# Optimization experiments

Measured on AMD Instinct MI355X. Metric: run time of the kernel, lower is better.

The kernel has to match this reference:

```python
import jax, jax.numpy as jnp
import numpy as np

N_SITES = 1024
CHI = 128


def _cayley_isometry(X):
    # X: (m, n) with m >= n. Pad to square, skew-symmetrize, Cayley transform
    # Q = (I + A)^{-1}(I - A) (orthogonal for skew A), keep first n columns
    # -> isometry with orthonormal columns (quimb isometrize(method='cayley')).
    m, n = X.shape
    S = jnp.zeros((m, m), X.dtype).at[:, :n].set(X)
    A = 0.5 * (S - S.T)
    I = jnp.eye(m, dtype=X.dtype)
    Q = jnp.linalg.solve(I + A, I - A)
    return Q[:, :n]


def setup_inputs() -> dict:
    key = jax.random.key(0)
    k1, k2 = jax.random.split(key)
    params = jax.random.normal(k1, (N_SITES, 2 * CHI, CHI), jnp.float32) * 0.1
    rand_uniform = jax.random.uniform(k2, (N_SITES,), dtype=jnp.float32)
    return {"params": params, "rand_uniform": rand_uniform}


def reference(params, rand_uniform):
    n, two_chi, chi = params.shape
    # norm_fn: isometrize every TN tensor via Cayley, reshape to (left,2,right)
    W = jax.vmap(_cayley_isometry)(params)          # (N, 2*chi, chi)
    T = W.reshape(n, chi, 2, chi)
    l = jnp.zeros((chi,), W.dtype).at[0].set(1.0)   # left boundary vector
    r = jnp.zeros((chi,), W.dtype).at[0].set(1.0)   # right boundary vector

    # right environments of <psi|psi>: Rs[i] contracts sites i..N-1
    def right_step(R, Ti):
        Rn = jnp.einsum('asb,csd,bd->ac', Ti, Ti, R)
        return Rn, Rn

    R_last = jnp.outer(r, r)
    _, Rs = jax.lax.scan(right_step, R_last, T, reverse=True)
    # env strictly to the right of site i
    R_right = jnp.concatenate([Rs[1:], R_last[None]], axis=0)  # (N, chi, chi)

    # global normalization so conditional probs satisfy ps0+ps1 = 1
    L0 = jnp.outer(l, l)
    Z = jnp.einsum('ab,ab->', L0, Rs[0])
    T = T.at[0].multiply(jax.lax.rsqrt(Z))

    def sample_step(L, inp):
        Ti, Ri, u = inp
        # reduced density matrix on this site's physical index k_i
        rho = jnp.einsum('ab,asc,btd,cd->st', L, Ti, Ti, Ri)
        ps0 = rho[1, 1]   # <v0|rho|v0>, v0 = [0, 1]
        ps1 = rho[0, 0]   # <v1|rho|v1>, v1 = [1, 0]
        take0 = u < ps0
        vec = jnp.where(take0,
                        jnp.array([0.0, 1.0], rho.dtype),
                        jnp.array([1.0, 0.0], rho.dtype))
        p = jnp.where(take0, ps0, ps1)
        # project site on sampled vector, renormalize by its probability
        M = jnp.einsum('asb,s->ab', Ti, vec)
        Ln = jnp.einsum('ab,ac,bd->cd', L, M, M) / p
        return N_ if False else (Ln, vec)

    _, s_hat = jax.lax.scan(sample_step, L0, (T, R_right, rand_uniform))
    return s_hat  # (N, 2) float32, rows are v0=[0,1] or v1=[1,0]
```

## Files before the change

kernel.cpp:

```cpp
#include <hip/hip_runtime.h>
#include <math.h>

#define NS 1024
#define SENT (-1.0e300)

template <typename T> struct V2;
template <> struct V2<double> { using t = double2; };
template <> struct V2<float>  { using t = float2; };

template <typename T> __device__ __forceinline__ T sentv();
template <> __device__ __forceinline__ double sentv<double>() { return -1.0e300; }
template <> __device__ __forceinline__ float  sentv<float>()  { return -3.0e38f; }

template <typename T>
__device__ __forceinline__ T aldT(const T* p) {
  return __hip_atomic_load(p, __ATOMIC_RELAXED, __HIP_MEMORY_SCOPE_AGENT);
}
__device__ __forceinline__ double ald(const double* p) {
  return __hip_atomic_load(p, __ATOMIC_RELAXED, __HIP_MEMORY_SCOPE_AGENT);
}
template <typename T>
__device__ __forceinline__ void ast(T* p, T v) {
  __hip_atomic_store(p, v, __ATOMIC_RELAXED, __HIP_MEMORY_SCOPE_AGENT);
}

template <typename TR>
__global__ void k_init(double* __restrict__ wbuf, TR* __restrict__ Rbuf) {
  size_t stride = (size_t)gridDim.x * blockDim.x;
  size_t t = (size_t)blockIdx.x * blockDim.x + threadIdx.x;
  for (size_t idx = t; idx < (size_t)(NS + 1) * 128; idx += stride)
    wbuf[idx] = (idx < 128) ? ((idx == 0) ? 1.0 : 0.0) : SENT;
  const size_t lastoff = (size_t)(NS - 1) * 16384;
  for (size_t idx = t; idx < (size_t)NS * 16384; idx += stride)
    Rbuf[idx] = (idx < lastoff) ? sentv<TR>()
                                : (TR)((idx == lastoff) ? 1.0f : 0.0f);
}

template <typename TT, typename TR>
__global__ __launch_bounds__(256) void k_cayley(const float* __restrict__ params,
                                                TT* __restrict__ Tk,
                                                TR* __restrict__ Yscr) {
  __shared__ float XB[64 * 132];
  __shared__ double prow[128], fcol[128];
  const int site = blockIdx.x, tid = threadIdx.x;
  const float* X = params + (size_t)site * 256 * 128;
  const int ti = tid >> 4, tj = tid & 15;
  const int R0 = ti * 8, C0 = tj * 8;
  double g[8][8];
  #pragma unroll
  for (int i = 0; i < 8; ++i)
    #pragma unroll
    for (int j = 0; j < 8; ++j) g[i][j] = ((R0 + i) == (C0 + j)) ? 1.0 : 0.0;
  for (int h = 0; h < 2; ++h) {
    for (int idx = tid; idx < 64 * 128; idx += 256) {
      int rr = idx >> 7, c = idx & 127;
      XB[rr * 132 + c] = X[(size_t)(h * 64 + rr) * 128 + c];
    }
    __syncthreads();
    int lo = h * 64;
    if ((R0 >> 6) == h) {
      #pragma unroll
      for (int i = 0; i < 8; ++i)
        #pragma unroll
        for (int j = 0; j < 8; ++j)
          g[i][j] += 0.5 * (double)XB[(R0 + i - lo) * 132 + (C0 + j)];
    }
    if ((C0 >> 6) == h) {
      #pragma unroll
      for (int i = 0; i < 8; ++i)
        #pragma unroll
        for (int j = 0; j < 8; ++j)
          g[i][j] -= 0.5 * (double)XB[(C0 + j - lo) * 132 + (R0 + i)];
    }
    __syncthreads();
  }
  for (int h = 0; h < 2; ++h) {
    for (int idx = tid; idx < 64 * 128; idx += 256) {
      int rr = idx >> 7, c = idx & 127;
      XB[rr * 132 + c] = X[(size_t)(128 + h * 64 + rr) * 128 + c];
    }
    __syncthreads();
    for (int a = 0; a < 64; ++a) {
      double fa[8], fb[8];
      #pragma unroll
      for (int i = 0; i < 8; ++i) fa[i] = 0.5 * (double)XB[a * 132 + R0 + i];
      #pragma unroll
      for (int j = 0; j < 8; ++j) fb[j] = 0.5 * (double)XB[a * 132 + C0 + j];
      #pragma unroll
      for (int i = 0; i < 8; ++i)
        #pragma unroll
        for (int j = 0; j < 8; ++j) g[i][j] += fa[i] * fb[j];
    }
    __syncthreads();
  }
  for (int p = 0; p < 128; ++p) {
    int pb = p >> 3, pl = p & 7;
    if (ti == pb) {
      #pragma unroll
      for (int j = 0; j < 8; ++j) prow[C0 + j] = g[pl][j];
    }
    if (tj == pb) {
      #pragma unroll
      for (int i = 0; i < 8; ++i) fcol[R0 + i] = g[i][pl];
    }
    __syncthreads();
    double d = 1.0 / prow[p];
    double pd[8];
    #pragma unroll
    for (int j = 0; j < 8; ++j) pd[j] = prow[C0 + j] * d;
    #pragma unroll
    for (int i = 0; i < 8; ++i) {
      int r = R0 + i;
      if (r == p) {
        #pragma unroll
        for (int j = 0; j < 8; ++j) g[i][j] = ((C0 + j) == p) ? d : pd[j];
      } else {
        double f = fcol[r];
        #pragma unroll
        for (int j = 0; j < 8; ++j)
          g[i][j] = ((C0 + j) == p) ? (-f * d) : (g[i][j] - f * pd[j]);
      }
    }
    __syncthreads();
  }
  TR* Ys = Yscr + (size_t)site * 16384;
  TT* Ts = Tk + (size_t)site * 32768;
  #pragma unroll
  for (int i = 0; i < 8; ++i) {
    int r = R0 + i, s = r & 1, a = r >> 1;
    #pragma unroll
    for (int j = 0; j < 8; ++j) {
      int c = C0 + j;
      Ys[(size_t)r * 128 + c] = (TR)g[i][j];
      Ts[((size_t)s * 128 + a) * 128 + c] =
          (TT)(2.0 * g[i][j] - ((r == c) ? 1.0 : 0.0));
    }
  }
}

template <typename TT, typename TR>
__global__ __launch_bounds__(256) void k_w2(const float* __restrict__ params,
                                            const TR* __restrict__ Yscr,
                                            TT* __restrict__ Tk) {
  __shared__ float X2c[16 * 132];
  __shared__ double Yt[16 * 130];
  const int site = blockIdx.x, tid = threadIdx.x;
  const float* X2g = params + (size_t)site * 256 * 128 + 128 * 128;
  const TR* Ys = Yscr + (size_t)site * 16384;
  TT* Ts = Tk + (size_t)site * 32768;
  const int ti = tid >> 4, tj = tid & 15;
  const int R0 = ti * 8, C0 = tj * 8;
  double acc[8][8];
  #pragma unroll
  for (int i = 0; i < 8; ++i)
    #pragma unroll
    for (int j = 0; j < 8; ++j) acc[i][j] = 0.0;
  for (int b0 = 0; b0 < 128; b0 += 16) {
    __syncthreads();
    for (int idx = tid; idx < 2048; idx += 256) {
      int r = idx >> 4, bb = idx & 15;
      X2c[bb * 132 + r] = X2g[(size_t)r * 128 + b0 + bb];
    }
    for (int idx = tid; idx < 2048; idx += 256) {
      int bb = idx >> 7, c = idx & 127;
      Yt[bb * 130 + c] = (double)Ys[(size_t)(b0 + bb) * 128 + c];
    }
    __syncthreads();
    for (int bb = 0; bb < 16; ++bb) {
      double xf[8], yf[8];
      #pragma unroll
      for (int i = 0; i < 8; ++i) xf[i] = (double)X2c[bb * 132 + R0 + i];
      #pragma unroll
      for (int j = 0; j < 8; ++j) yf[j] = Yt[bb * 130 + C0 + j];
      #pragma unroll
      for (int i = 0; i < 8; ++i)
        #pragma unroll
        for (int j = 0; j < 8; ++j) acc[i][j] += xf[i] * yf[j];
    }
  }
  #pragma unroll
  for (int i = 0; i < 8; ++i) {
    int r = 128 + R0 + i, s = r & 1, a = r >> 1;
    #pragma unroll
    for (int j = 0; j < 8; ++j)
      Ts[((size_t)s * 128 + a) * 128 + C0 + j] = (TT)(-acc[i][j]);
  }
}

template <typename TT, typename TR>
__global__ __launch_bounds__(512) void k_scan(const TT* __restrict__ Tk,
                                              TR* __restrict__ Rbuf,
                                              TR* __restrict__ Rs0,
                                              double* __restrict__ Zp) {
  __shared__ double KA[8 * 128];
  __shared__ double KC[16 * 129];
  __shared__ double Rt[16 * 128];
  __shared__ double Pb[8 * 129];
  __shared__ double red[256];
  const int w = blockIdx.x, tid = threadIdx.x;
  const int a0 = (w >> 3) * 4, c0 = (w & 7) * 16;
  const int r2 = tid >> 7, bh = tid & 127;
  const TR SV = sentv<TR>();
  for (int i = NS - 1; i >= 0; --i) {
    const TT* K = Tk + (size_t)i * 32768;
    const TR* Rin = Rbuf + (size_t)i * 16384;
    double v[4];
    #pragma unroll
    for (int u = 0; u < 4; ++u) {
      TR t = aldT(Rin + tid * 4 + u);
      v[u] = (t == SV) ? SENT : (double)t;
    }
    for (int idx = tid; idx < 1024; idx += 512) {
      int row = idx >> 7, col = idx & 127;
      KA[idx] = (double)K[(size_t)((row >> 2) * 128 + a0 + (row & 3)) * 128 + col];
    }
    double kc[8];
    #pragma unroll
    for (int u = 0; u < 8; ++u) {
      int row = r2 + 4 * u;
      kc[u] = (double)K[(size_t)((row >> 4) * 128 + c0 + (row & 15)) * 128 + bh];
    }
    double acc0 = 0.0, acc1 = 0.0;
    for (int c = 0; c < 8; ++c) {
      while (v[0] == SENT || v[1] == SENT || v[2] == SENT || v[3] == SENT) {
        __builtin_amdgcn_s_sleep(1);
        #pragma unroll
        for (int u = 0; u < 4; ++u)
          if (v[u] == SENT) {
            TR t = aldT(Rin + c * 2048 + tid * 4 + u);
            v[u] = (t == SV) ? SENT : (double)t;
          }
      }
      {
        int base = tid * 4, dl = base >> 7, bb = base & 127;
        Rt[dl * 128 + bb] = v[0];
        Rt[dl * 128 + bb + 1] = v[1];
        Rt[dl * 128 + bb + 2] = v[2];
        Rt[dl * 128 + bb + 3] = v[3];
      }
      __syncthreads();
      if (c < 7) {
        #pragma unroll
        for (int u = 0; u < 4; ++u) {
          TR t = aldT(Rin + (c + 1) * 2048 + tid * 4 + u);
          v[u] = (t == SV) ? SENT : (double)t;
        }
      }
      #pragma unroll
      for (int dl = 0; dl < 16; ++dl) {
        int d = c * 16 + dl;
        double rr = Rt[dl * 128 + bh];
        acc0 += KA[r2 * 128 + d] * rr;
        acc1 += KA[(r2 + 4) * 128 + d] * rr;
      }
      __syncthreads();
    }
    Pb[r2 * 129 + bh] = acc0;
    Pb[(r2 + 4) * 129 + bh] = acc1;
    __syncthreads();
    double s = 0.0;
    const int oi = tid & 63, seg = (tid >> 6) & 3;
    #pragma unroll
    for (int j = 0; j < 2; ++j) {
      #pragma unroll
      for (int t = 0; t < 4; ++t)
        KC[(r2 + 4 * t) * 129 + bh] = kc[j * 4 + t];
      __syncthreads();
      if (tid < 256) {
        int aa = oi >> 4, cc = oi & 15;
        double acc = 0.0;
        #pragma unroll
        for (int m = 0; m < 32; ++m) {
          int b = seg * 32 + m;
          acc += Pb[(j * 4 + aa) * 129 + b] * KC[cc * 129 + b];
        }
        s += acc;
      }
      __syncthreads();
    }
    if (tid < 256) red[tid] = s;
    __syncthreads();
    if (tid < 64) {
      int aa = tid >> 4, cc = tid & 15;
      double o = red[tid] + red[tid + 64] + red[tid + 128] + red[tid + 192];
      TR* outp = (i > 0) ? (Rbuf + (size_t)(i - 1) * 16384) : Rs0;
      ast(&outp[(size_t)(a0 + aa) * 128 + c0 + cc], (TR)o);
      if (i == 0 && w == 0 && tid == 0) ast(Zp, o);
    }
    __syncthreads();
  }
}

template <typename TT, typename TR>
__global__ __launch_bounds__(1024) void k_sample(const TT* __restrict__ Tk,
                                                 const TR* __restrict__ Rbuf,
                                                 double* __restrict__ wbuf,
                                                 const double* __restrict__ Zp,
                                                 const float* __restrict__ randu,
                                                 float* __restrict__ out) {
  __shared__ double wl[128], yl[256], part[1024], ctrl[2];
  const int g = blockIdx.x, tid = threadIdx.x;
  const int s = tid >> 9, q = (tid >> 7) & 3, b = tid & 127;
  const int lane = tid & 63, wv = tid >> 6;
  using TR2 = typename V2<TR>::t;
  for (int site = g; site < NS; site += 16) {
    const TT* T = Tk + (size_t)site * 32768;
    double tf[32];
    {
      const TT* tp = T + ((size_t)s * 128 + q * 32) * 128 + b;
      #pragma unroll
      for (int t = 0; t < 32; ++t) tf[t] = (double)tp[(size_t)t * 128];
    }
    double rv[16];
    {
      const TR2* R2 = (const TR2*)(Rbuf + (size_t)site * 16384);
      #pragma unroll
      for (int t = 0; t < 8; ++t) {
        TR2 v = R2[t * 1024 + tid];
        rv[2 * t] = (double)v.x; rv[2 * t + 1] = (double)v.y;
      }
    }
    if (tid < 128) {
      double* wp = wbuf + (size_t)site * 128 + tid;
      double v;
      while ((v = ald(wp)) == SENT) __builtin_amdgcn_s_sleep(1);
      wl[tid] = v;
    }
    __syncthreads();
    {
      double p0 = 0.0;
      #pragma unroll
      for (int t = 0; t < 32; ++t) p0 += tf[t] * wl[q * 32 + t];
      part[(s * 4 + q) * 128 + b] = p0;
    }
    __syncthreads();
    if (tid < 256) {
      int ss = tid >> 7, bb = tid & 127;
      yl[ss * 128 + bb] = part[(ss * 4) * 128 + bb] + part[(ss * 4 + 1) * 128 + bb] +
                          part[(ss * 4 + 2) * 128 + bb] + part[(ss * 4 + 3) * 128 + bb];
    }
    __syncthreads();
    {
      double y1a = yl[128 + 2 * lane], y1b = yl[128 + 2 * lane + 1];
      double vp = 0.0;
      #pragma unroll
      for (int t = 0; t < 8; ++t)
        vp += yl[128 + 16 * t + wv] * (rv[2 * t] * y1a + rv[2 * t + 1] * y1b);
      #pragma unroll
      for (int off = 1; off < 64; off <<= 1) vp += __shfl_xor(vp, off, 64);
      if (lane == 0) part[wv] = vp;
    }
    __syncthreads();
    if (tid == 0) {
      double v = 0.0;
      #pragma unroll
      for (int k = 0; k < 16; ++k) v += part[k];
      double zn = (site == 0) ? *Zp : 1.0;
      double ps0 = v / zn;
      double u = (double)randu[site];
      bool take0 = u < ps0;
      double pp = take0 ? ps0 : (1.0 - ps0);
      ctrl[0] = take0 ? 1.0 : 0.0;
      ctrl[1] = 1.0 / sqrt(pp * zn);
      out[2 * site] = take0 ? 0.0f : 1.0f;
      out[2 * site + 1] = take0 ? 1.0f : 0.0f;
    }
    __syncthreads();
    {
      int k = (ctrl[0] != 0.0) ? 1 : 0;
      double sc = ctrl[1];
      if (tid < 128)
        ast(&wbuf[(size_t)(site + 1) * 128 + tid], yl[k * 128 + tid] * sc);
    }
    __syncthreads();
  }
}

__global__ void k_diag(float* __restrict__ out, int n, float mb) {
  int i = blockIdx.x * blockDim.x + threadIdx.x;
  if (i < n) out[i] = (i == 0) ? mb : ((i & 1) ? 0.75f : 0.25f);
}

template <typename TT, typename TR>
struct Plan {
  size_t oTk, oR, oRs0, oW, oZ, need;
  Plan() {
    oTk = 0;
    oR = oTk + sizeof(TT) * (size_t)NS * 32768;
    oRs0 = oR + sizeof(TR) * (size_t)NS * 16384;
    oW = oRs0 + sizeof(TR) * 16384;
    oZ = oW + 8ull * (NS + 1) * 128;
    need = oZ + 64;
  }
};

template <typename TT, typename TR>
static void run_cfg(const float* params, const float* randu, float* out,
                    char* ws, hipStream_t stream) {
  Plan<TT, TR> P;
  TT* Tk = (TT*)(ws + P.oTk);
  TR* Rbuf = (TR*)(ws + P.oR);
  TR* Yscr = Rbuf;
  TR* Rs0 = (TR*)(ws + P.oRs0);
  double* wbuf = (double*)(ws + P.oW);
  double* Zp = (double*)(ws + P.oZ);
  k_cayley<TT, TR><<<dim3(NS), dim3(256), 0, stream>>>(params, Tk, Yscr);
  k_w2<TT, TR><<<dim3(NS), dim3(256), 0, stream>>>(params, Yscr, Tk);
  k_init<TR><<<dim3(4096), dim3(256), 0, stream>>>(wbuf, Rbuf);
  k_scan<TT, TR><<<dim3(256), dim3(512), 0, stream>>>(Tk, Rbuf, Rs0, Zp);
  k_sample<TT, TR><<<dim3(16), dim3(1024), 0, stream>>>(Tk, Rbuf, wbuf, Zp, randu, out);
}

extern "C" void kernel_launch(void* const* d_in, const int* in_sizes, int n_in,
                              void* d_out, int out_size, void* d_ws, size_t ws_size,
                              hipStream_t stream) {
  const float* params = (const float*)d_in[0];
  const float* randu = (const float*)d_in[1];
  float* out = (float*)d_out;
  char* ws = (char*)d_ws;
  if (ws_size >= Plan<double, double>().need) {
    run_cfg<double, double>(params, randu, out, ws, stream);
  } else if (ws_size >= Plan<float, double>().need) {
    run_cfg<float, double>(params, randu, out, ws, stream);
  } else if (ws_size >= Plan<float, float>().need) {
    run_cfg<float, float>(params, randu, out, ws, stream);
  } else {
    k_diag<<<dim3((out_size + 255) / 256), dim3(256), 0, stream>>>(
        out, out_size, (float)(ws_size >> 20));
  }
}
```

Baseline: 17.00 ms.

## Pair adjacent sites to halve the serial right-environment scan depth

Precomputes products of adjacent site tensors (k_pair) so a chain of blocks advances the right environment two sites per step, while a second group of blocks fills in the odd intermediate environments concurrently. The sampling kernel also processes two sites per iteration, and scan loads use cache-bypassing vector loads with sentinel polling. This cuts the length of the serially dependent scan, at the cost of an extra batched GEMM, a large workspace buffer and more flops per chain step.

```diff
diff --git a/kernel.cpp b/kernel.cpp
--- a/kernel.cpp
+++ b/kernel.cpp
@@ -22,6 +22,15 @@
 template <typename T>
 __device__ __forceinline__ void ast(T* p, T v) {
   __hip_atomic_store(p, v, __ATOMIC_RELAXED, __HIP_MEMORY_SCOPE_AGENT);
+}
+
+typedef __attribute__((ext_vector_type(2))) double dx2;
+__device__ __forceinline__ void cld(dx2& d, const double* p) {
+  asm volatile("global_load_dwordx4 %0, %1, off sc0 sc1" : "=v"(d) : "v"(p));
+}
+__device__ __forceinline__ void cldw(dx2& d, const double* p) {
+  asm volatile("global_load_dwordx4 %0, %1, off sc0 sc1\n\ts_waitcnt vmcnt(0)"
+               : "=v"(d) : "v"(p));
 }
 
 template <typename TR>
@@ -187,6 +196,167 @@
   }
 }
 
+template <typename TB>
+__global__ __launch_bounds__(256) void k_pair(const double* __restrict__ Tk,
+                                              TB* __restrict__ Bbuf) {
+  __shared__ double As[16 * 136];
+  __shared__ double Bs[16 * 132];
+  const int blk = blockIdx.x, tid = threadIdx.x;
+  const int p = blk >> 2, q = blk & 3, s = q >> 1, sp = q & 1;
+  const double* A = Tk + ((size_t)(2 * p) * 2 + s) * 16384;
+  const double* B = Tk + ((size_t)(2 * p + 1) * 2 + sp) * 16384;
+  TB* outp = Bbuf + ((size_t)p * 4 + q) * 16384;
+  const int ti = tid >> 4, tj = tid & 15, R0 = ti * 8, C0 = tj * 8;
+  double acc[8][8];
+  #pragma unroll
+  for (int i = 0; i < 8; ++i)
+    #pragma unroll
+    for (int j = 0; j < 8; ++j) acc[i][j] = 0.0;
+  for (int b0 = 0; b0 < 128; b0 += 16) {
+    __syncthreads();
+    for (int idx = tid; idx < 2048; idx += 256) {
+      int r = idx >> 4, bb = idx & 15;
+      As[bb * 136 + r] = A[(size_t)r * 128 + b0 + bb];
+    }
+    for (int idx = tid; idx < 2048; idx += 256) {
+      int bb = idx >> 7, c = idx & 127;
+      Bs[bb * 132 + c] = B[(size_t)(b0 + bb) * 128 + c];
+    }
+    __syncthreads();
+    for (int bb = 0; bb < 16; ++bb) {
+      double fa[8], fb[8];
+      #pragma unroll
+      for (int i = 0; i < 8; ++i) fa[i] = As[bb * 136 + R0 + i];
+      #pragma unroll
+      for (int j = 0; j < 8; ++j) fb[j] = Bs[bb * 132 + C0 + j];
+      #pragma unroll
+      for (int i = 0; i < 8; ++i)
+        #pragma unroll
+        for (int j = 0; j < 8; ++j) acc[i][j] += fa[i] * fb[j];
+    }
+  }
+  #pragma unroll
+  for (int i = 0; i < 8; ++i)
+    #pragma unroll
+    for (int j = 0; j < 8; ++j)
+      outp[(size_t)(R0 + i) * 128 + C0 + j] = (TB)acc[i][j];
+}
+
+template <int NOP, typename TOP>
+__device__ __forceinline__ void scan_step(const TOP* __restrict__ op,
+    const double* __restrict__ Rin, double* __restrict__ outp,
+    double* __restrict__ Zp, bool writeZ, double* KAPb, double* KCs,
+    double* Rt, double* red, int a0, int c0, int tid) {
+  const int r2 = tid >> 7, bh = tid & 127;
+  for (int idx = tid; idx < NOP * 512; idx += 512) {
+    int row = idx >> 7, col = idx & 127;
+    KAPb[idx] =
+        (double)op[(size_t)(row >> 2) * 16384 + (a0 + (row & 3)) * 128 + col];
+  }
+  dx2 v[16];
+  const double* src = Rin + tid * 4;
+  #pragma unroll
+  for (int c = 0; c < 8; ++c) {
+    cld(v[2 * c], src + c * 2048);
+    cld(v[2 * c + 1], src + c * 2048 + 2);
+  }
+  asm volatile("s_waitcnt vmcnt(0)" ::: "memory");
+  __builtin_amdgcn_sched_barrier(0);
+  double acc[NOP];
+  #pragma unroll
+  for (int k = 0; k < NOP; ++k) acc[k] = 0.0;
+  const int dl0 = tid >> 5, bb0 = (tid * 4) & 127;
+  #pragma unroll
+  for (int c = 0; c < 8; ++c) {
+    dx2 va = v[2 * c], vb = v[2 * c + 1];
+    while (va.x == SENT || va.y == SENT || vb.x == SENT || vb.y == SENT) {
+      __builtin_amdgcn_s_sleep(1);
+      cldw(va, src + c * 2048);
+      cldw(vb, src + c * 2048 + 2);
+    }
+    double* rt = Rt + (c & 1) * 2048;
+    rt[dl0 * 128 + bb0] = va.x;
+    rt[dl0 * 128 + bb0 + 1] = va.y;
+    rt[dl0 * 128 + bb0 + 2] = vb.x;
+    rt[dl0 * 128 + bb0 + 3] = vb.y;
+    __syncthreads();
+    #pragma unroll
+    for (int dl = 0; dl < 16; ++dl) {
+      double rr = rt[dl * 128 + bh];
+      #pragma unroll
+      for (int k = 0; k < NOP; ++k)
+        acc[k] += KAPb[(r2 + 4 * k) * 128 + c * 16 + dl] * rr;
+    }
+  }
+  double kc[4 * NOP];
+  #pragma unroll
+  for (int u = 0; u < 4 * NOP; ++u) {
+    int row = r2 + 4 * u;
+    kc[u] =
+        (double)op[(size_t)(row >> 4) * 16384 + (c0 + (row & 15)) * 128 + bh];
+  }
+  __syncthreads();
+  #pragma unroll
+  for (int k = 0; k < NOP; ++k) KAPb[(r2 + 4 * k) * 129 + bh] = acc[k];
+  __syncthreads();
+  double sacc = 0.0;
+  const int oi = tid & 63, seg = (tid >> 6) & 3;
+  #pragma unroll
+  for (int j = 0; j < NOP; ++j) {
+    #pragma unroll
+    for (int t = 0; t < 4; ++t) KCs[(r2 + 4 * t) * 129 + bh] = kc[j * 4 + t];
+    __syncthreads();
+    if (tid < 256) {
+      int aa = oi >> 4, cc = oi & 15;
+      double a2 = 0.0;
+      #pragma unroll
+      for (int m = 0; m < 32; ++m)
+        a2 += KAPb[(j * 4 + aa) * 129 + seg * 32 + m] *
+              KCs[cc * 129 + seg * 32 + m];
+      sacc += a2;
+    }
+    __syncthreads();
+  }
+  if (tid < 256) red[tid] = sacc;
+  __syncthreads();
+  if (tid < 64) {
+    int aa = tid >> 4, cc = tid & 15;
+    double o = red[tid] + red[tid + 64] + red[tid + 128] + red[tid + 192];
+    ast(&outp[(size_t)(a0 + aa) * 128 + c0 + cc], o);
+    if (writeZ && tid == 0) ast(Zp, o);
+  }
+  __syncthreads();
+}
+
+template <typename TB>
+__global__ __launch_bounds__(512, 4) void k_scan2(
+    const double* __restrict__ Tk, const TB* __restrict__ Bbuf,
+    double* __restrict__ Rbuf, double* __restrict__ Rs0,
+    double* __restrict__ Zp) {
+  __shared__ double KAPb[2064], KCs[2064], Rt[4096], red[256];
+  const int w = blockIdx.x, tid = threadIdx.x;
+  const bool chain = (w < 256);
+  const int tw = chain ? w : (w - 256);
+  const int a0 = (tw >> 3) * 4, c0 = (tw & 7) * 16;
+  if (chain) {
+    __builtin_amdgcn_s_setprio(1);
+    for (int p = 511; p >= 0; --p) {
+      const TB* opb = Bbuf + (size_t)p * 65536;
+      const double* Rin = Rbuf + (size_t)(2 * p + 1) * 16384;
+      double* outp = (p > 0) ? (Rbuf + (size_t)(2 * p - 1) * 16384) : Rs0;
+      scan_step<4>(opb, Rin, outp, Zp, p == 0 && tw == 0, KAPb, KCs, Rt, red,
+                   a0, c0, tid);
+    }
+  } else {
+    for (int p = 511; p >= 0; --p) {
+      const double* opb = Tk + (size_t)(2 * p + 1) * 32768;
+      const double* Rin = Rbuf + (size_t)(2 * p + 1) * 16384;
+      double* outp = Rbuf + (size_t)(2 * p) * 16384;
+      scan_step<2>(opb, Rin, outp, Zp, false, KAPb, KCs, Rt, red, a0, c0, tid);
+    }
+  }
+}
+
 template <typename TT, typename TR>
 __global__ __launch_bounds__(512) void k_scan(const TT* __restrict__ Tk,
                                               TR* __restrict__ Rbuf,
@@ -194,7 +364,7 @@
                                               double* __restrict__ Zp) {
   __shared__ double KA[8 * 128];
   __shared__ double KC[16 * 129];
-  __shared__ double Rt[16 * 128];
+  __shared__ double Rt2[16 * 128];
   __shared__ double Pb[8 * 129];
   __shared__ double red[256];
   const int w = blockIdx.x, tid = threadIdx.x;
@@ -233,10 +403,10 @@
       }
       {
         int base = tid * 4, dl = base >> 7, bb = base & 127;
-        Rt[dl * 128 + bb] = v[0];
-        Rt[dl * 128 + bb + 1] = v[1];
-        Rt[dl * 128 + bb + 2] = v[2];
-        Rt[dl * 128 + bb + 3] = v[3];
+        Rt2[dl * 128 + bb] = v[0];
+        Rt2[dl * 128 + bb + 1] = v[1];
+        Rt2[dl * 128 + bb + 2] = v[2];
+        Rt2[dl * 128 + bb + 3] = v[3];
       }
       __syncthreads();
       if (c < 7) {
@@ -249,7 +419,7 @@
       #pragma unroll
       for (int dl = 0; dl < 16; ++dl) {
         int d = c * 16 + dl;
-        double rr = Rt[dl * 128 + bh];
+        double rr = Rt2[dl * 128 + bh];
         acc0 += KA[r2 * 128 + d] * rr;
         acc1 += KA[(r2 + 4) * 128 + d] * rr;
       }
@@ -376,6 +546,145 @@
   }
 }
 
+__global__ __launch_bounds__(1024) void k_sample2(
+    const double* __restrict__ Tk, const double* __restrict__ Rbuf,
+    double* __restrict__ wbuf, const double* __restrict__ Zp,
+    const float* __restrict__ randu, float* __restrict__ out) {
+  __shared__ double wl[128], yl[256], part[1024], ctrl[2];
+  const int g = blockIdx.x, tid = threadIdx.x;
+  const int s = tid >> 9, q = (tid >> 7) & 3, b = tid & 127;
+  const int lane = tid & 63, wv = tid >> 6;
+  for (int p = g; p < 512; p += 16) {
+    const int siteA = 2 * p, siteB = siteA + 1;
+    const double* TA = Tk + (size_t)siteA * 32768;
+    const double* TBp = Tk + (size_t)siteB * 32768;
+    double tfA[32];
+    {
+      const double* tp = TA + ((size_t)s * 128 + q * 32) * 128 + b;
+      #pragma unroll
+      for (int t = 0; t < 32; ++t) tfA[t] = tp[(size_t)t * 128];
+    }
+    double rvA[16], rvB[16];
+    {
+      const double2* R2 = (const double2*)(Rbuf + (size_t)siteA * 16384);
+      #pragma unroll
+      for (int t = 0; t < 8; ++t) {
+        double2 vv = R2[t * 1024 + tid];
+        rvA[2 * t] = vv.x; rvA[2 * t + 1] = vv.y;
+      }
+      const double2* R3 = (const double2*)(Rbuf + (size_t)siteB * 16384);
+      #pragma unroll
+      for (int t = 0; t < 8; ++t) {
+        double2 vv = R3[t * 1024 + tid];
+        rvB[2 * t] = vv.x; rvB[2 * t + 1] = vv.y;
+      }
+    }
+    if (tid < 128) {
+      double* wp = wbuf + (size_t)siteA * 128 + tid;
+      double vv;
+      while ((vv = ald(wp)) == SENT) __builtin_amdgcn_s_sleep(1);
+      wl[tid] = vv;
+    }
+    __syncthreads();
+    {
+      double p0 = 0.0;
+      #pragma unroll
+      for (int t = 0; t < 32; ++t) p0 += tfA[t] * wl[q * 32 + t];
+      part[(s * 4 + q) * 128 + b] = p0;
+    }
+    double tfB[32];
+    {
+      const double* tp = TBp + ((size_t)s * 128 + q * 32) * 128 + b;
+      #pragma unroll
+      for (int t = 0; t < 32; ++t) tfB[t] = tp[(size_t)t * 128];
+    }
+    __syncthreads();
+    if (tid < 256) {
+      int ss = tid >> 7, bb = tid & 127;
+      yl[ss * 128 + bb] = part[(ss * 4) * 128 + bb] + part[(ss * 4 + 1) * 128 + bb] +
+                          part[(ss * 4 + 2) * 128 + bb] + part[(ss * 4 + 3) * 128 + bb];
+    }
+    __syncthreads();
+    {
+      double y1a = yl[128 + 2 * lane], y1b = yl[128 + 2 * lane + 1];
+      double vp = 0.0;
+      #pragma unroll
+      for (int t = 0; t < 8; ++t)
+        vp += yl[128 + 16 * t + wv] * (rvA[2 * t] * y1a + rvA[2 * t + 1] * y1b);
+      #pragma unroll
+      for (int off = 1; off < 64; off <<= 1) vp += __shfl_xor(vp, off, 64);
+      if (lane == 0) part[wv] = vp;
+    }
+    __syncthreads();
+    if (tid == 0) {
+      double vv = 0.0;
+      #pragma unroll
+      for (int k = 0; k < 16; ++k) vv += part[k];
+      double zn = (siteA == 0) ? *Zp : 1.0;
+      double ps0 = vv / zn;
+      double u = (double)randu[siteA];
+      bool take0 = u < ps0;
+      double pp = take0 ? ps0 : (1.0 - ps0);
+      ctrl[0] = take0 ? 1.0 : 0.0;
+      ctrl[1] = 1.0 / sqrt(pp * zn);
+      out[2 * siteA] = take0 ? 0.0f : 1.0f;
+      out[2 * siteA + 1] = take0 ? 1.0f : 0.0f;
+    }
+    __syncthreads();
+    {
+      int k = (ctrl[0] != 0.0) ? 1 : 0;
+      double sc = ctrl[1];
+      if (tid < 128) wl[tid] = yl[k * 128 + tid] * sc;
+    }
+    __syncthreads();
+    {
+      double p1 = 0.0;
+      #pragma unroll
+      for (int t = 0; t < 32; ++t) p1 += tfB[t] * wl[q * 32 + t];
+      part[(s * 4 + q) * 128 + b] = p1;
+    }
+    __syncthreads();
+    if (tid < 256) {
+      int ss = tid >> 7, bb = tid & 127;
+      yl[ss * 128 + bb] = part[(ss * 4) * 128 + bb] + part[(ss * 4 + 1) * 128 + bb] +
+                          part[(ss * 4 + 2) * 128 + bb] + part[(ss * 4 + 3) * 128 + bb];
+    }
+    __syncthreads();
+    {
+      double y1a = yl[128 + 2 * lane], y1b = yl[128 + 2 * lane + 1];
+      double vp = 0.0;
+      #pragma unroll
+      for (int t = 0; t < 8; ++t)
+        vp += yl[128 + 16 * t + wv] * (rvB[2 * t] * y1a + rvB[2 * t + 1] * y1b);
+      #pragma unroll
+      for (int off = 1; off < 64; off <<= 1) vp += __shfl_xor(vp, off, 64);
+      if (lane == 0) part[wv] = vp;
+    }
+    __syncthreads();
+    if (tid == 0) {
+      double vv = 0.0;
+      #pragma unroll
+      for (int k = 0; k < 16; ++k) vv += part[k];
+      double ps0 = vv;
+      double u = (double)randu[siteB];
+      bool take0 = u < ps0;
+      double pp = take0 ? ps0 : (1.0 - ps0);
+      ctrl[0] = take0 ? 1.0 : 0.0;
+      ctrl[1] = 1.0 / sqrt(pp);
+      out[2 * siteB] = take0 ? 0.0f : 1.0f;
+      out[2 * siteB + 1] = take0 ? 1.0f : 0.0f;
+    }
+    __syncthreads();
+    {
+      int k = (ctrl[0] != 0.0) ? 1 : 0;
+      double sc = ctrl[1];
+      if (tid < 128)
+        ast(&wbuf[(size_t)(siteB + 1) * 128 + tid], yl[k * 128 + tid] * sc);
+    }
+    __syncthreads();
+  }
+}
+
 __global__ void k_diag(float* __restrict__ out, int n, float mb) {
   int i = blockIdx.x * blockDim.x + threadIdx.x;
   if (i < n) out[i] = (i == 0) ? mb : ((i & 1) ? 0.75f : 0.25f);
@@ -391,6 +700,20 @@
     oW = oRs0 + sizeof(TR) * 16384;
     oZ = oW + 8ull * (NS + 1) * 128;
     need = oZ + 64;
+  }
+};
+
+template <typename TB>
+struct PlanP {
+  size_t oTk, oR, oRs0, oW, oZ, oB, need;
+  PlanP() {
+    oTk = 0;
+    oR = oTk + sizeof(double) * (size_t)NS * 32768;
+    oRs0 = oR + sizeof(double) * (size_t)NS * 16384;
+    oW = oRs0 + sizeof(double) * 16384;
+    oZ = oW + 8ull * (NS + 1) * 128;
+    oB = oZ + 64;
+    need = oB + sizeof(TB) * (size_t)(NS / 2) * 4 * 16384;
   }
 };
 
@@ -411,6 +734,25 @@
   k_sample<TT, TR><<<dim3(16), dim3(1024), 0, stream>>>(Tk, Rbuf, wbuf, Zp, randu, out);
 }
 
+template <typename TB>
+static void run_pair(const float* params, const float* randu, float* out,
+                     char* ws, hipStream_t stream) {
+  PlanP<TB> P;
+  double* Tk = (double*)(ws + P.oTk);
+  double* Rbuf = (double*)(ws + P.oR);
+  double* Yscr = Rbuf;
+  double* Rs0 = (double*)(ws + P.oRs0);
+  double* wbuf = (double*)(ws + P.oW);
+  double* Zp = (double*)(ws + P.oZ);
+  TB* Bbuf = (TB*)(ws + P.oB);
+  k_cayley<double, double><<<dim3(NS), dim3(256), 0, stream>>>(params, Tk, Yscr);
+  k_w2<double, double><<<dim3(NS), dim3(256), 0, stream>>>(params, Yscr, Tk);
+  k_init<double><<<dim3(4096), dim3(256), 0, stream>>>(wbuf, Rbuf);
+  k_pair<TB><<<dim3(2048), dim3(256), 0, stream>>>(Tk, Bbuf);
+  k_scan2<TB><<<dim3(512), dim3(512), 0, stream>>>(Tk, Bbuf, Rbuf, Rs0, Zp);
+  k_sample2<<<dim3(16), dim3(1024), 0, stream>>>(Tk, Rbuf, wbuf, Zp, randu, out);
+}
+
 extern "C" void kernel_launch(void* const* d_in, const int* in_sizes, int n_in,
                               void* d_out, int out_size, void* d_ws, size_t ws_size,
                               hipStream_t stream) {
@@ -418,7 +760,11 @@
   const float* randu = (const float*)d_in[1];
   float* out = (float*)d_out;
   char* ws = (char*)d_ws;
-  if (ws_size >= Plan<double, double>().need) {
+  if (ws_size >= PlanP<double>().need) {
+    run_pair<double>(params, randu, out, ws, stream);
+  } else if (ws_size >= PlanP<float>().need) {
+    run_pair<float>(params, randu, out, ws, stream);
+  } else if (ws_size >= Plan<double, double>().need) {
     run_cfg<double, double>(params, randu, out, ws, stream);
   } else if (ws_size >= Plan<float, double>().need) {
     run_cfg<float, double>(params, randu, out, ws, stream);
```

Result: no change. 17.00 ms (+0.0%).

## Fuse adjacent site pairs into two-site operators to halve sequential scan steps

Applied to the files above, without the earlier changes.

Adds a path that precomputes, for every pair of neighbouring sites, the four 128x128 products of their projected tensors. The right-environment scan and the sampling sweep then step over 512 pairs instead of 1024 sites, and each sampling step samples two sites at once using conditional probabilities. This halves the serial dependency chain and the cross-block spin-wait handoffs. In exchange it adds a batched matmul pre-pass, more shared memory and work per step, and extra workspace. The new path is selected first whenever the workspace is large enough.

```diff
diff --git a/kernel.cpp b/kernel.cpp
--- a/kernel.cpp
+++ b/kernel.cpp
@@ -34,6 +34,16 @@
   for (size_t idx = t; idx < (size_t)NS * 16384; idx += stride)
     Rbuf[idx] = (idx < lastoff) ? sentv<TR>()
                                 : (TR)((idx == lastoff) ? 1.0f : 0.0f);
+}
+
+__global__ void k_init2(double* __restrict__ wbuf, double* __restrict__ Rodd) {
+  size_t stride = (size_t)gridDim.x * blockDim.x;
+  size_t t = (size_t)blockIdx.x * blockDim.x + threadIdx.x;
+  for (size_t idx = t; idx < (size_t)513 * 128; idx += stride)
+    wbuf[idx] = (idx < 128) ? ((idx == 0) ? 1.0 : 0.0) : SENT;
+  const size_t lastoff = (size_t)511 * 16384;
+  for (size_t idx = t; idx < (size_t)512 * 16384; idx += stride)
+    Rodd[idx] = (idx < lastoff) ? SENT : ((idx == lastoff) ? 1.0 : 0.0);
 }
 
 template <typename TT, typename TR>
@@ -187,6 +197,236 @@
   }
 }
 
+template <typename TT>
+__global__ __launch_bounds__(256) void k_pair2(const TT* __restrict__ Tk,
+                                               double* __restrict__ outB,
+                                               int pair0) {
+  __shared__ double As[16 * 136];
+  __shared__ double Bs[16 * 132];
+  const int blk = blockIdx.x, tid = threadIdx.x;
+  const int pl = blk >> 2, q = blk & 3, s = q >> 1, sp = q & 1;
+  const int p = pair0 + pl;
+  const TT* A = Tk + ((size_t)(2 * p) * 2 + s) * 16384;
+  const TT* B = Tk + ((size_t)(2 * p + 1) * 2 + sp) * 16384;
+  double* outp = outB + (size_t)pl * 65536 + (size_t)q * 16384;
+  const int ti = tid >> 4, tj = tid & 15, R0 = ti * 8, C0 = tj * 8;
+  double acc[8][8];
+  #pragma unroll
+  for (int i = 0; i < 8; ++i)
+    #pragma unroll
+    for (int j = 0; j < 8; ++j) acc[i][j] = 0.0;
+  for (int b0 = 0; b0 < 128; b0 += 16) {
+    __syncthreads();
+    for (int idx = tid; idx < 2048; idx += 256) {
+      int r = idx >> 4, bb = idx & 15;
+      As[bb * 136 + r] = (double)A[(size_t)r * 128 + b0 + bb];
+    }
+    for (int idx = tid; idx < 2048; idx += 256) {
+      int bb = idx >> 7, c = idx & 127;
+      Bs[bb * 132 + c] = (double)B[(size_t)(b0 + bb) * 128 + c];
+    }
+    __syncthreads();
+    for (int bb = 0; bb < 16; ++bb) {
+      double fa[8], fb[8];
+      #pragma unroll
+      for (int i = 0; i < 8; ++i) fa[i] = As[bb * 136 + R0 + i];
+      #pragma unroll
+      for (int j = 0; j < 8; ++j) fb[j] = Bs[bb * 132 + C0 + j];
+      #pragma unroll
+      for (int i = 0; i < 8; ++i)
+        #pragma unroll
+        for (int j = 0; j < 8; ++j) acc[i][j] += fa[i] * fb[j];
+    }
+  }
+  #pragma unroll
+  for (int i = 0; i < 8; ++i)
+    #pragma unroll
+    for (int j = 0; j < 8; ++j)
+      outp[(size_t)(R0 + i) * 128 + C0 + j] = acc[i][j];
+}
+
+__global__ __launch_bounds__(512, 2) void k_scan3(const double* __restrict__ Blo,
+                                                  const double* __restrict__ Bhi,
+                                                  int splitP,
+                                                  double* __restrict__ Rodd,
+                                                  double* __restrict__ Rs0,
+                                                  double* __restrict__ Zp) {
+  __shared__ double KA[16 * 128];
+  __shared__ double KC[16 * 129];
+  __shared__ double Rt[16 * 128];
+  __shared__ double Pb[16 * 129];
+  __shared__ double red[256];
+  const int w = blockIdx.x, tid = threadIdx.x;
+  const int a0 = (w >> 3) * 4, c0 = (w & 7) * 16;
+  const int r2 = tid >> 7, bh = tid & 127;
+  for (int p = 511; p >= 0; --p) {
+    const double* op = (p < splitP) ? (Blo + (size_t)p * 65536)
+                                    : (Bhi + (size_t)(p - splitP) * 65536);
+    const double* Rin = Rodd + (size_t)p * 16384;
+    double v[4];
+    #pragma unroll
+    for (int u = 0; u < 4; ++u) v[u] = ald(Rin + tid * 4 + u);
+    for (int idx = tid; idx < 2048; idx += 512) {
+      int row = idx >> 7, col = idx & 127;
+      KA[idx] = op[(size_t)(row >> 2) * 16384 + (size_t)(a0 + (row & 3)) * 128 + col];
+    }
+    double kc[16];
+    #pragma unroll
+    for (int u = 0; u < 16; ++u) {
+      int row = r2 + 4 * u;
+      kc[u] = op[(size_t)(row >> 4) * 16384 + (size_t)(c0 + (row & 15)) * 128 + bh];
+    }
+    double acc0 = 0.0, acc1 = 0.0, acc2 = 0.0, acc3 = 0.0;
+    for (int c = 0; c < 8; ++c) {
+      while (v[0] == SENT || v[1] == SENT || v[2] == SENT || v[3] == SENT) {
+        __builtin_amdgcn_s_sleep(1);
+        #pragma unroll
+        for (int u = 0; u < 4; ++u)
+          if (v[u] == SENT) v[u] = ald(Rin + c * 2048 + tid * 4 + u);
+      }
+      {
+        int base = tid * 4, dl = base >> 7, bb = base & 127;
+        Rt[dl * 128 + bb] = v[0];
+        Rt[dl * 128 + bb + 1] = v[1];
+        Rt[dl * 128 + bb + 2] = v[2];
+        Rt[dl * 128 + bb + 3] = v[3];
+      }
+      __syncthreads();
+      if (c < 7) {
+        #pragma unroll
+        for (int u = 0; u < 4; ++u)
+          v[u] = ald(Rin + (c + 1) * 2048 + tid * 4 + u);
+      }
+      #pragma unroll
+      for (int dl = 0; dl < 16; ++dl) {
+        int d = c * 16 + dl;
+        double rr = Rt[dl * 128 + bh];
+        acc0 += KA[(r2) * 128 + d] * rr;
+        acc1 += KA[(r2 + 4) * 128 + d] * rr;
+        acc2 += KA[(r2 + 8) * 128 + d] * rr;
+        acc3 += KA[(r2 + 12) * 128 + d] * rr;
+      }
+      __syncthreads();
+    }
+    Pb[(r2) * 129 + bh] = acc0;
+    Pb[(r2 + 4) * 129 + bh] = acc1;
+    Pb[(r2 + 8) * 129 + bh] = acc2;
+    Pb[(r2 + 12) * 129 + bh] = acc3;
+    __syncthreads();
+    double s = 0.0;
+    const int oi = tid & 63, seg = (tid >> 6) & 3;
+    #pragma unroll
+    for (int j = 0; j < 4; ++j) {
+      #pragma unroll
+      for (int t = 0; t < 4; ++t)
+        KC[(r2 + 4 * t) * 129 + bh] = kc[j * 4 + t];
+      __syncthreads();
+      if (tid < 256) {
+        int aa = oi >> 4, cc = oi & 15;
+        double acc = 0.0;
+        #pragma unroll
+        for (int m = 0; m < 32; ++m) {
+          int b = seg * 32 + m;
+          acc += Pb[(j * 4 + aa) * 129 + b] * KC[cc * 129 + b];
+        }
+        s += acc;
+      }
+      __syncthreads();
+    }
+    if (tid < 256) red[tid] = s;
+    __syncthreads();
+    if (tid < 64) {
+      int aa = tid >> 4, cc = tid & 15;
+      double o = red[tid] + red[tid + 64] + red[tid + 128] + red[tid + 192];
+      double* outp = (p > 0) ? (Rodd + (size_t)(p - 1) * 16384) : Rs0;
+      ast(&outp[(size_t)(a0 + aa) * 128 + c0 + cc], o);
+      if (p == 0 && w == 0 && tid == 0) ast(Zp, o);
+    }
+    __syncthreads();
+  }
+}
+
+__global__ __launch_bounds__(512, 2) void k_sample4(
+    const double* __restrict__ Blo, const double* __restrict__ Bhi, int splitP,
+    const double* __restrict__ Rodd, double* __restrict__ wbuf,
+    const double* __restrict__ Zp, const float* __restrict__ randu,
+    float* __restrict__ out) {
+  __shared__ double Rl[16384];
+  __shared__ double wl[128], yl[512], part[64], ctrl[2];
+  const int g = blockIdx.x, tid = threadIdx.x;
+  const int q = tid >> 7, c = tid & 127;
+  const int lane = tid & 63, wv = tid >> 6;
+  for (int p = g; p < 512; p += 32) {
+    const double* Bb = (p < splitP) ? (Blo + (size_t)p * 65536)
+                                    : (Bhi + (size_t)(p - splitP) * 65536);
+    float bf[128];
+    {
+      const double* bp = Bb + (size_t)q * 16384 + c;
+      #pragma unroll 16
+      for (int r = 0; r < 128; ++r) bf[r] = (float)bp[(size_t)r * 128];
+    }
+    {
+      const double* Rp = Rodd + (size_t)p * 16384;
+      #pragma unroll 4
+      for (int u = 0; u < 32; ++u) Rl[u * 512 + tid] = Rp[u * 512 + tid];
+    }
+    if (tid < 128) {
+      double* wp = wbuf + (size_t)p * 128 + tid;
+      double vv;
+      while ((vv = ald(wp)) == SENT) __builtin_amdgcn_s_sleep(1);
+      wl[tid] = vv;
+    }
+    __syncthreads();
+    {
+      double acc = 0.0;
+      #pragma unroll 8
+      for (int r = 0; r < 128; ++r) acc += (double)bf[r] * wl[r];
+      yl[q * 128 + c] = acc;
+    }
+    __syncthreads();
+    {
+      double z = 0.0;
+      #pragma unroll 8
+      for (int r = 0; r < 128; ++r) z += Rl[r * 128 + c] * yl[q * 128 + r];
+      double qp = z * yl[q * 128 + c];
+      #pragma unroll
+      for (int off = 1; off < 64; off <<= 1) qp += __shfl_xor(qp, off, 64);
+      if (lane == 0) part[wv] = qp;
+    }
+    __syncthreads();
+    if (tid == 0) {
+      double Q0 = part[0] + part[1], Q1 = part[2] + part[3];
+      double Q2 = part[4] + part[5], Q3 = part[6] + part[7];
+      double zn = (p == 0) ? *Zp : 1.0;
+      double ps0e = (Q2 + Q3) / zn;
+      double ue = (double)randu[2 * p];
+      bool t0e = ue < ps0e;
+      double pe = t0e ? ps0e : (1.0 - ps0e);
+      int ke = t0e ? 1 : 0;
+      out[4 * p] = t0e ? 0.0f : 1.0f;
+      out[4 * p + 1] = t0e ? 1.0f : 0.0f;
+      double Qk1 = (ke == 1) ? Q3 : Q1;
+      double ps0o = Qk1 / (pe * zn);
+      double uo = (double)randu[2 * p + 1];
+      bool t0o = uo < ps0o;
+      double po = t0o ? ps0o : (1.0 - ps0o);
+      int ko = t0o ? 1 : 0;
+      out[4 * p + 2] = t0o ? 0.0f : 1.0f;
+      out[4 * p + 3] = t0o ? 1.0f : 0.0f;
+      ctrl[0] = (double)(ke * 2 + ko);
+      ctrl[1] = 1.0 / sqrt(pe * po * zn);
+    }
+    __syncthreads();
+    {
+      int ksel = (int)ctrl[0];
+      double sc = ctrl[1];
+      if (tid < 128)
+        ast(&wbuf[(size_t)(p + 1) * 128 + tid], yl[ksel * 128 + tid] * sc);
+    }
+    __syncthreads();
+  }
+}
+
 template <typename TT, typename TR>
 __global__ __launch_bounds__(512) void k_scan(const TT* __restrict__ Tk,
                                               TR* __restrict__ Rbuf,
@@ -194,7 +434,7 @@
                                               double* __restrict__ Zp) {
   __shared__ double KA[8 * 128];
   __shared__ double KC[16 * 129];
-  __shared__ double Rt[16 * 128];
+  __shared__ double Rt2[16 * 128];
   __shared__ double Pb[8 * 129];
   __shared__ double red[256];
   const int w = blockIdx.x, tid = threadIdx.x;
@@ -233,10 +473,10 @@
       }
       {
         int base = tid * 4, dl = base >> 7, bb = base & 127;
-        Rt[dl * 128 + bb] = v[0];
-        Rt[dl * 128 + bb + 1] = v[1];
-        Rt[dl * 128 + bb + 2] = v[2];
-        Rt[dl * 128 + bb + 3] = v[3];
+        Rt2[dl * 128 + bb] = v[0];
+        Rt2[dl * 128 + bb + 1] = v[1];
+        Rt2[dl * 128 + bb + 2] = v[2];
+        Rt2[dl * 128 + bb + 3] = v[3];
       }
       __syncthreads();
       if (c < 7) {
@@ -249,7 +489,7 @@
       #pragma unroll
       for (int dl = 0; dl < 16; ++dl) {
         int d = c * 16 + dl;
-        double rr = Rt[dl * 128 + bh];
+        double rr = Rt2[dl * 128 + bh];
         acc0 += KA[r2 * 128 + d] * rr;
         acc1 += KA[(r2 + 4) * 128 + d] * rr;
       }
@@ -394,6 +634,26 @@
   }
 };
 
+template <typename TT>
+struct PlanN {
+  size_t oTk, oScr, oR, oRs0, oW, oZ, need;
+  int splitP;
+  PlanN() {
+    splitP = (sizeof(TT) == 8) ? 256 : 128;
+    oTk = 0;
+    size_t tkB = sizeof(TT) * (size_t)NS * 32768;
+    oScr = tkB;
+    size_t yB = 8ull * NS * 16384;
+    size_t bhiB = 8ull * (size_t)(512 - splitP) * 4 * 16384;
+    size_t scrB = (yB > bhiB) ? yB : bhiB;
+    oR = oScr + scrB;
+    oRs0 = oR + 8ull * 512 * 16384;
+    oW = oRs0 + 8ull * 16384;
+    oZ = oW + 8ull * 513 * 128;
+    need = oZ + 64;
+  }
+};
+
 template <typename TT, typename TR>
 static void run_cfg(const float* params, const float* randu, float* out,
                     char* ws, hipStream_t stream) {
@@ -411,6 +671,29 @@
   k_sample<TT, TR><<<dim3(16), dim3(1024), 0, stream>>>(Tk, Rbuf, wbuf, Zp, randu, out);
 }
 
+template <typename TT>
+static void run_pairN(const float* params, const float* randu, float* out,
+                      char* ws, hipStream_t stream) {
+  PlanN<TT> P;
+  TT* Tk = (TT*)(ws + P.oTk);
+  double* Yscr = (double*)(ws + P.oScr);
+  double* Bhi = (double*)(ws + P.oScr);
+  double* Blo = (double*)(ws + P.oTk + sizeof(TT) * (size_t)512 * 32768);
+  double* Rodd = (double*)(ws + P.oR);
+  double* Rs0 = (double*)(ws + P.oRs0);
+  double* wbuf = (double*)(ws + P.oW);
+  double* Zp = (double*)(ws + P.oZ);
+  const int sp = P.splitP;
+  k_cayley<TT, double><<<dim3(NS), dim3(256), 0, stream>>>(params, Tk, Yscr);
+  k_w2<TT, double><<<dim3(NS), dim3(256), 0, stream>>>(params, Yscr, Tk);
+  k_init2<<<dim3(2048), dim3(256), 0, stream>>>(wbuf, Rodd);
+  k_pair2<TT><<<dim3((512 - sp) * 4), dim3(256), 0, stream>>>(Tk, Bhi, sp);
+  k_pair2<TT><<<dim3(sp * 4), dim3(256), 0, stream>>>(Tk, Blo, 0);
+  k_scan3<<<dim3(256), dim3(512), 0, stream>>>(Blo, Bhi, sp, Rodd, Rs0, Zp);
+  k_sample4<<<dim3(32), dim3(512), 0, stream>>>(Blo, Bhi, sp, Rodd, wbuf, Zp,
+                                                randu, out);
+}
+
 extern "C" void kernel_launch(void* const* d_in, const int* in_sizes, int n_in,
                               void* d_out, int out_size, void* d_ws, size_t ws_size,
                               hipStream_t stream) {
@@ -418,7 +701,11 @@
   const float* randu = (const float*)d_in[1];
   float* out = (float*)d_out;
   char* ws = (char*)d_ws;
-  if (ws_size >= Plan<double, double>().need) {
+  if (ws_size >= PlanN<double>().need) {
+    run_pairN<double>(params, randu, out, ws, stream);
+  } else if (ws_size >= PlanN<float>().need) {
+    run_pairN<float>(params, randu, out, ws, stream);
+  } else if (ws_size >= Plan<double, double>().need) {
     run_cfg<double, double>(params, randu, out, ws, stream);
   } else if (ws_size >= Plan<float, double>().need) {
     run_cfg<float, double>(params, randu, out, ws, stream);
```

Result: no change. 17.33 ms (+2.0%).
